# Kernel optimization log

Hardware: AMD Instinct MI355X
Metric: run time of the kernel (lower is better)

## Reference

```python
import jax, jax.numpy as jnp
import numpy as np

B, N, D, K, NUM_CLASSES = 8, 2048, 256, 8, 32
BN_EPS = 1e-5


def l2norm(x):
    return x / jnp.maximum(jnp.linalg.norm(x, axis=-1, keepdims=True), 1e-12)


def mlp2(x, W1, b1, W2, b2):
    # get_mlp([3, 32, D]): Linear -> ReLU -> Linear -> ReLU
    return jax.nn.relu(jax.nn.relu(x @ W1 + b1) @ W2 + b2)


def bn(x, g, b):
    # training-mode BatchNorm1d over all edges (flattened leading dims)
    ax = tuple(range(x.ndim - 1))
    m = jnp.mean(x, axis=ax, keepdims=True)
    v = jnp.var(x, axis=ax, keepdims=True)
    return (x - m) * jax.lax.rsqrt(v + BN_EPS) * g + b


def setup_inputs() -> dict:
    key = jax.random.key(0)
    ks = jax.random.split(key, 24)
    p = lambda i, shape: jax.random.normal(ks[i], shape, jnp.float32) * 0.05
    class_table = p(0, (NUM_CLASSES, D)).at[0].set(0.0)  # padding_idx=0
    return dict(
        class_idx=jax.random.randint(ks[1], (B, N), 0, NUM_CLASSES),
        colors=jax.random.uniform(ks[2], (B, N, 3), jnp.float32),
        positions=jax.random.normal(ks[3], (B, N, 3), jnp.float32),
        class_table=class_table,
        pos_W1=p(4, (3, 32)), pos_b1=p(5, (32,)),
        pos_W2=p(6, (32, D)), pos_b2=p(7, (D,)),
        col_W1=p(8, (3, 32)), col_b1=p(9, (32,)),
        col_W2=p(10, (32, D)), col_b2=p(11, (D,)),
        merge_W=p(12, (3 * D, D)), merge_b=p(13, (D,)),
        g_W1=p(14, (2 * D, D)), g_b1=p(15, (D,)),
        g_g1=jnp.ones((D,), jnp.float32), g_be1=jnp.zeros((D,), jnp.float32),
        g_W2=p(16, (D, D)), g_b2=p(17, (D,)),
        g_g2=jnp.ones((D,), jnp.float32), g_be2=jnp.zeros((D,), jnp.float32),
        lin_W1=p(18, (D, D)), lin_b1=p(19, (D,)),
        lin_W2=p(20, (D, D)), lin_b2=p(21, (D,)),
    )


def reference(class_idx, colors, positions, class_table,
              pos_W1, pos_b1, pos_W2, pos_b2,
              col_W1, col_b1, col_W2, col_b2,
              merge_W, merge_b,
              g_W1, g_b1, g_g1, g_be1, g_W2, g_b2, g_g2, g_be2,
              lin_W1, lin_b1, lin_W2, lin_b2):
    # --- per-object feature embeddings, each L2-normalized ---
    ce = l2norm(class_table[class_idx])                                   # [B,N,D]
    col = l2norm(mlp2(colors, col_W1, col_b1, col_W2, col_b2))            # [B,N,D]
    pos = l2norm(mlp2(positions, pos_W1, pos_b1, pos_W2, pos_b2))         # [B,N,D]
    x = jax.nn.relu(jnp.concatenate([ce, col, pos], -1) @ merge_W + merge_b)  # [B,N,D]
    # --- dynamic kNN in feature space, per sample (self edge included) ---
    sq = jnp.sum(x * x, -1)                                               # [B,N]
    d = sq[:, :, None] + sq[:, None, :] - 2.0 * jnp.einsum('bid,bjd->bij', x, x)
    _, idx = jax.lax.top_k(-jax.lax.stop_gradient(d), K)                  # [B,N,K]
    xj = jax.vmap(lambda e, i: e[i])(x, idx)                              # [B,N,K,D]
    xi = jnp.broadcast_to(x[:, :, None, :], xj.shape)
    e = jnp.concatenate([xi, xj - xi], -1)                                # [B,N,K,2D]
    # --- edge MLP [2D,D,D] with BN, max aggregation over neighbors ---
    h = bn(jax.nn.relu(e @ g_W1 + g_b1), g_g1, g_be1)
    h = bn(jax.nn.relu(h @ g_W2 + g_b2), g_g2, g_be2)
    node = jnp.max(h, axis=2)                                             # [B,N,D]
    pooled = jnp.max(node, axis=1)                                        # global_max_pool -> [B,D]
    out = jax.nn.relu(jax.nn.relu(pooled @ lin_W1 + lin_b1) @ lin_W2 + lin_b2)
    return l2norm(out)
```

## Files before the change

kernel.cpp:

```cpp
#include <hip/hip_runtime.h>
#include <math.h>

#define BB 8
#define NN 2048
#define DD 256
#define KNN 8
#define NPTS (BB*NN)
#define NEDGE (NPTS*KNN)
#define BN_EPS 1e-5f
#define NSH 64
#define PSH 32

#define OFF_X      0
#define OFF_FEAT   (OFF_X + NPTS*DD)
#define OFF_STATS  (OFF_FEAT + NPTS*3*DD)
#define OFF_PMAXS  (OFF_STATS + NSH*1024)
#define OFF_SQ     (OFF_PMAXS + PSH*BB*DD)
#define OFF_PMINS  (OFF_SQ + NPTS)
#define OFF_IDX    (OFF_PMINS + PSH*BB*DD)
#define OFF_U      (OFF_IDX + NEDGE)
#define OFF_V      (OFF_U + NPTS*DD)
#define OFF_W2BF   (OFF_V + NPTS*DD)
#define OFF_BIASP  (OFF_W2BF + 32768)
#define OFF_XHI    (OFF_BIASP + DD)
#define OFF_XLO    (OFF_XHI + NPTS*DD/2)
#define OFF_MWH    (OFF_XLO + NPTS*DD/2)
#define OFF_MWL    (OFF_MWH + 98304)
#define OFF_WUH    (OFF_MWL + 98304)
#define OFF_WUL    (OFF_WUH + 32768)
#define OFF_WBH    (OFF_WUL + 32768)
#define OFF_WBL    (OFF_WBH + 32768)

typedef __attribute__((ext_vector_type(8))) short bf16x8;
typedef __attribute__((ext_vector_type(4))) float f32x4;

__device__ __forceinline__ unsigned short f2bf(float f) {
  unsigned int u = __float_as_uint(f);
  u += 0x7FFF + ((u >> 16) & 1);
  return (unsigned short)(u >> 16);
}
__device__ __forceinline__ float bf2f(unsigned short h) {
  return __uint_as_float((unsigned int)h << 16);
}

__global__ __launch_bounds__(256) void prepk(
    const int* __restrict__ cls, const float* __restrict__ colors, const float* __restrict__ positions,
    const float* __restrict__ ctab,
    const float* __restrict__ pW1, const float* __restrict__ pb1, const float* __restrict__ pW2, const float* __restrict__ pb2,
    const float* __restrict__ cW1, const float* __restrict__ cb1, const float* __restrict__ cW2, const float* __restrict__ cb2,
    unsigned short* __restrict__ feathi, unsigned short* __restrict__ featlo,
    const float* __restrict__ mW,
    unsigned short* __restrict__ mwh, unsigned short* __restrict__ mwl,
    const float* __restrict__ gW1,
    unsigned short* __restrict__ Wuh, unsigned short* __restrict__ Wul,
    unsigned short* __restrict__ Wbh, unsigned short* __restrict__ Wbl)
{
  __shared__ float wbuf[4][64];
  int bx = blockIdx.x;
  int tid = threadIdx.x;
  if (bx < 4096) {
    int wv = tid >> 6, lane = tid & 63;
    int p = bx*4 + wv;
    if (lane < 32) {
      float c0 = colors[p*3+0], c1 = colors[p*3+1], c2 = colors[p*3+2];
      wbuf[wv][lane] = fmaxf(c0*cW1[lane] + c1*cW1[32+lane] + c2*cW1[64+lane] + cb1[lane], 0.f);
    } else {
      int l = lane - 32;
      float q0 = positions[p*3+0], q1 = positions[p*3+1], q2 = positions[p*3+2];
      wbuf[wv][32+l] = fmaxf(q0*pW1[l] + q1*pW1[32+l] + q2*pW1[64+l] + pb1[l], 0.f);
    }
    __syncthreads();
    int c = lane*4;
    float4 ce4 = *(const float4*)&ctab[(size_t)cls[p]*DD + c];
    float4 col4 = *(const float4*)&cb2[c];
    float4 pos4 = *(const float4*)&pb2[c];
    #pragma unroll
    for (int k = 0; k < 32; k++) {
      float ch = wbuf[wv][k], ph = wbuf[wv][32+k];
      float4 cw = *(const float4*)&cW2[k*DD + c];
      float4 pw = *(const float4*)&pW2[k*DD + c];
      col4.x += ch*cw.x; col4.y += ch*cw.y; col4.z += ch*cw.z; col4.w += ch*cw.w;
      pos4.x += ph*pw.x; pos4.y += ph*pw.y; pos4.z += ph*pw.z; pos4.w += ph*pw.w;
    }
    col4.x = fmaxf(col4.x, 0.f); col4.y = fmaxf(col4.y, 0.f);
    col4.z = fmaxf(col4.z, 0.f); col4.w = fmaxf(col4.w, 0.f);
    pos4.x = fmaxf(pos4.x, 0.f); pos4.y = fmaxf(pos4.y, 0.f);
    pos4.z = fmaxf(pos4.z, 0.f); pos4.w = fmaxf(pos4.w, 0.f);
    float sce  = ce4.x*ce4.x + ce4.y*ce4.y + ce4.z*ce4.z + ce4.w*ce4.w;
    float scol = col4.x*col4.x + col4.y*col4.y + col4.z*col4.z + col4.w*col4.w;
    float spos = pos4.x*pos4.x + pos4.y*pos4.y + pos4.z*pos4.z + pos4.w*pos4.w;
    #pragma unroll
    for (int m = 1; m <= 32; m <<= 1) {
      sce  += __shfl_xor(sce,  m, 64);
      scol += __shfl_xor(scol, m, 64);
      spos += __shfl_xor(spos, m, 64);
    }
    float ice = 1.f / fmaxf(sqrtf(sce),  1e-12f);
    float icl = 1.f / fmaxf(sqrtf(scol), 1e-12f);
    float ips = 1.f / fmaxf(sqrtf(spos), 1e-12f);
    float o[3][4] = {
      {ce4.x*ice,  ce4.y*ice,  ce4.z*ice,  ce4.w*ice},
      {col4.x*icl, col4.y*icl, col4.z*icl, col4.w*icl},
      {pos4.x*ips, pos4.y*ips, pos4.z*ips, pos4.w*ips}
    };
    #pragma unroll
    for (int sgm = 0; sgm < 3; sgm++) {
      unsigned short h[4], l[4];
      #pragma unroll
      for (int cc = 0; cc < 4; cc++) {
        h[cc] = f2bf(o[sgm][cc]);
        l[cc] = f2bf(o[sgm][cc] - bf2f(h[cc]));
      }
      size_t off = (size_t)p*768 + sgm*256 + c;
      *(uint2*)&feathi[off] = make_uint2((unsigned)h[0] | ((unsigned)h[1] << 16),
                                         (unsigned)h[2] | ((unsigned)h[3] << 16));
      *(uint2*)&featlo[off] = make_uint2((unsigned)l[0] | ((unsigned)l[1] << 16),
                                         (unsigned)l[2] | ((unsigned)l[3] << 16));
    }
  } else if (bx < 4096 + 768) {
    int k = bx - 4096;
    int n = tid;
    float wgt = mW[(size_t)k*DD + n];
    unsigned short h = f2bf(wgt);
    mwh[(size_t)n*768 + k] = h;
    mwl[(size_t)n*768 + k] = f2bf(wgt - bf2f(h));
  } else {
    int k = bx - (4096 + 768);
    int n = tid;
    float t = gW1[(size_t)k*DD + n];
    float b = gW1[(size_t)(k + DD)*DD + n];
    float wu = t - b;
    unsigned short uh = f2bf(wu), bh = f2bf(b);
    Wuh[(size_t)n*DD + k] = uh;
    Wul[(size_t)n*DD + k] = f2bf(wu - bf2f(uh));
    Wbh[(size_t)n*DD + k] = bh;
    Wbl[(size_t)n*DD + k] = f2bf(b - bf2f(bh));
  }
}

__global__ __launch_bounds__(256) void gemm768(
    const unsigned short* __restrict__ feathi, const unsigned short* __restrict__ featlo,
    const unsigned short* __restrict__ mwh, const unsigned short* __restrict__ mwl,
    const float* __restrict__ mb,
    float* __restrict__ sqo,
    unsigned short* __restrict__ xhi, unsigned short* __restrict__ xlo)
{
  __shared__ float wSh[128*18];
  __shared__ float wSl[128*18];
  int tid = threadIdx.x;
  int w = tid >> 6, lane = tid & 63;
  int m = lane & 15, quad = lane >> 4;
  int rowbase = blockIdx.x * 64;
  int colbase = blockIdx.y * 128;
  size_t aoff = (size_t)(rowbase + w*16 + m)*768;
  int srow = tid >> 1;
  int sseg = (tid & 1) * 2;
  f32x4 acc[8];
  #pragma unroll
  for (int t = 0; t < 8; t++) acc[t] = (f32x4){0.f, 0.f, 0.f, 0.f};
  #pragma unroll 1
  for (int c = 0; c < 24; c++) {
    int k0 = c*32 + quad*8;
    bf16x8 ah = *(const bf16x8*)(feathi + aoff + k0);
    bf16x8 al = *(const bf16x8*)(featlo + aoff + k0);
    const float* wrh = (const float*)(mwh + (size_t)(colbase + srow)*768 + c*32);
    const float* wrl = (const float*)(mwl + (size_t)(colbase + srow)*768 + c*32);
    float4 wh0 = *(const float4*)(wrh + sseg*4);
    float4 wh1 = *(const float4*)(wrh + (sseg+1)*4);
    float4 wl0 = *(const float4*)(wrl + sseg*4);
    float4 wl1 = *(const float4*)(wrl + (sseg+1)*4);
    __syncthreads();
    *(float4*)&wSh[srow*18 + sseg*4]     = wh0;
    *(float4*)&wSh[srow*18 + (sseg+1)*4] = wh1;
    *(float4*)&wSl[srow*18 + sseg*4]     = wl0;
    *(float4*)&wSl[srow*18 + (sseg+1)*4] = wl1;
    __syncthreads();
    #pragma unroll
    for (int nt = 0; nt < 8; nt++) {
      bf16x8 bh = *(const bf16x8*)&wSh[(nt*16 + m)*18 + quad*4];
      bf16x8 bl = *(const bf16x8*)&wSl[(nt*16 + m)*18 + quad*4];
      acc[nt] = __builtin_amdgcn_mfma_f32_16x16x32_bf16(ah, bh, acc[nt], 0, 0, 0);
      acc[nt] = __builtin_amdgcn_mfma_f32_16x16x32_bf16(ah, bl, acc[nt], 0, 0, 0);
      acc[nt] = __builtin_amdgcn_mfma_f32_16x16x32_bf16(al, bh, acc[nt], 0, 0, 0);
    }
  }
  float sqp[4] = {0.f, 0.f, 0.f, 0.f};
  #pragma unroll
  for (int nt = 0; nt < 8; nt++) {
    int col = colbase + nt*16 + m;
    float bp = mb[col];
    #pragma unroll
    for (int r = 0; r < 4; r++) {
      float o = fmaxf(acc[nt][r] + bp, 0.f);
      int row = rowbase + w*16 + quad*4 + r;
      unsigned short h = f2bf(o);
      xhi[(size_t)row*DD + col] = h;
      xlo[(size_t)row*DD + col] = f2bf(o - bf2f(h));
      sqp[r] += o*o;
    }
  }
  #pragma unroll
  for (int r = 0; r < 4; r++) {
    #pragma unroll
    for (int mm = 1; mm <= 8; mm <<= 1) sqp[r] += __shfl_xor(sqp[r], mm, 64);
  }
  if (m == 0) {
    #pragma unroll
    for (int r = 0; r < 4; r++)
      atomicAdd(&sqo[rowbase + w*16 + quad*4 + r], sqp[r]);
  }
}

__global__ __launch_bounds__(256) void knnuv(
    const unsigned short* __restrict__ xhi, const unsigned short* __restrict__ xlo,
    const float* __restrict__ sq,
    float* __restrict__ pdg, int* __restrict__ pjg,
    const unsigned short* __restrict__ Wuh, const unsigned short* __restrict__ Wul,
    const unsigned short* __restrict__ Wbh, const unsigned short* __restrict__ Wbl,
    float* __restrict__ U, float* __restrict__ V)
{
  __shared__ float smem[4736];
  int bx = blockIdx.x;
  int tid = threadIdx.x;
  int w = tid >> 6, lane = tid & 63;
  int m = lane & 15, quad = lane >> 4;
  if ((bx & 1) == 0) {
    int kid = bx >> 1;
    float* jh = smem;
    float* jl = smem + 2304;
    float (*dt)[65] = (float(*)[65])smem;
    float* sqI = smem + 4608;
    float* sqJ = smem + 4672;
    int q  = kid & 3;
    int it = (kid >> 2) & 31;
    int bb = kid >> 7;
    int ibase = it * 64;
    const unsigned short* xhb = xhi + (size_t)bb*NN*DD;
    const unsigned short* xlb = xlo + (size_t)bb*NN*DD;
    const float* sqb = sq + (size_t)bb*NN;
    int selrow = tid & 63, selseg = tid >> 6;
    size_t aoff = (size_t)(ibase + w*16 + m)*DD;
    int srow = tid >> 2;
    int sseg = tid & 3;
    bf16x8 ahr[8], alr[8];
    #pragma unroll
    for (int c = 0; c < 8; c++) {
      int k0 = c*32 + quad*8;
      ahr[c] = *(const bf16x8*)(xhb + aoff + k0);
      alr[c] = *(const bf16x8*)(xlb + aoff + k0);
    }
    float bd[8]; int bj[8];
    #pragma unroll
    for (int s = 0; s < 8; s++) { bd[s] = 3.4e38f; bj[s] = 0; }
    if (tid < 64) sqI[tid] = sqb[ibase + tid];
    #pragma unroll 1
    for (int jt = 0; jt < 8; jt++) {
      int jbase = q*512 + jt*64;
      if (tid < 64) sqJ[tid] = sqb[jbase + tid];
      f32x4 acc[4];
      #pragma unroll
      for (int t = 0; t < 4; t++) acc[t] = (f32x4){0.f, 0.f, 0.f, 0.f};
      #pragma unroll
      for (int c2 = 0; c2 < 4; c2++) {
        size_t gb = (size_t)(jbase + srow)*DD + c2*64;
        float4 h0 = *(const float4*)((const float*)(xhb + gb) + sseg*4);
        float4 h1 = *(const float4*)((const float*)(xhb + gb) + (sseg+4)*4);
        float4 l0 = *(const float4*)((const float*)(xlb + gb) + sseg*4);
        float4 l1 = *(const float4*)((const float*)(xlb + gb) + (sseg+4)*4);
        __syncthreads();
        *(float4*)&jh[srow*36 + sseg*4]     = h0;
        *(float4*)&jh[srow*36 + (sseg+4)*4] = h1;
        *(float4*)&jl[srow*36 + sseg*4]     = l0;
        *(float4*)&jl[srow*36 + (sseg+4)*4] = l1;
        __syncthreads();
        #pragma unroll
        for (int kk = 0; kk < 2; kk++) {
          bf16x8 ah = ahr[c2*2 + kk];
          bf16x8 al = alr[c2*2 + kk];
          int lofs = kk*16 + quad*4;
          #pragma unroll
          for (int nt = 0; nt < 4; nt++) {
            int r = nt*16 + m;
            bf16x8 bh = *(const bf16x8*)&jh[r*36 + lofs];
            bf16x8 bl = *(const bf16x8*)&jl[r*36 + lofs];
            acc[nt] = __builtin_amdgcn_mfma_f32_16x16x32_bf16(ah, bh, acc[nt], 0, 0, 0);
            acc[nt] = __builtin_amdgcn_mfma_f32_16x16x32_bf16(ah, bl, acc[nt], 0, 0, 0);
            acc[nt] = __builtin_amdgcn_mfma_f32_16x16x32_bf16(al, bh, acc[nt], 0, 0, 0);
          }
        }
      }
      __syncthreads();
      #pragma unroll
      for (int nt = 0; nt < 4; nt++) {
        int col = nt*16 + m;
        float sj = sqJ[col];
        #pragma unroll
        for (int r = 0; r < 4; r++) {
          int rowl = w*16 + quad*4 + r;
          dt[rowl][col] = sqI[rowl] + sj - 2.f*acc[nt][r];
        }
      }
      __syncthreads();
      int cb = selseg*16;
      #pragma unroll
      for (int s = 0; s < 16; s++) {
        float dv = dt[selrow][cb + s];
        if (dv < bd[7]) {
          bd[7] = dv; bj[7] = jbase + cb + s;
          #pragma unroll
          for (int t = 7; t >= 1; t--) {
            if (bd[t] < bd[t-1]) {
              float td = bd[t]; bd[t] = bd[t-1]; bd[t-1] = td;
              int   tj = bj[t]; bj[t] = bj[t-1]; bj[t-1] = tj;
            }
          }
        }
      }
    }
    __syncthreads();
    float* pdl = &smem[0];
    int*   pjl = (int*)&smem[2048];
    #pragma unroll
    for (int s = 0; s < 8; s++) {
      pdl[tid*8 + s] = bd[s];
      pjl[tid*8 + s] = bj[s];
    }
    __syncthreads();
    if (tid < 64) {
      float md[8]; int mj[8];
      #pragma unroll
      for (int s = 0; s < 8; s++) { md[s] = 3.4e38f; mj[s] = 0; }
      #pragma unroll 1
      for (int g = 0; g < 4; g++) {
        int base = (g*64 + tid)*8;
        #pragma unroll
        for (int s = 0; s < 8; s++) {
          float dv = pdl[base + s];
          if (dv < md[7]) {
            md[7] = dv; mj[7] = pjl[base + s];
            #pragma unroll
            for (int t = 7; t >= 1; t--) {
              if (md[t] < md[t-1]) {
                float td = md[t]; md[t] = md[t-1]; md[t-1] = td;
                int   tj = mj[t]; mj[t] = mj[t-1]; mj[t-1] = tj;
              }
            }
          }
        }
      }
      size_t gbase = ((size_t)(bb*NN + ibase + tid))*32 + (size_t)q*8;
      #pragma unroll
      for (int s = 0; s < 8; s++) {
        pdg[gbase + s] = md[s];
        pjg[gbase + s] = bb*NN + mj[s];
      }
    }
  } else {
    int gid = bx >> 1;
    float* wSh = smem;
    float* wSl = smem + 2304;
    int rowbase = (gid & 255) * 64;
    int yy = gid >> 8;
    int uv = yy >> 1;
    int colbase = (yy & 1) * 128;
    const unsigned short* Wh = uv ? Wbh : Wuh;
    const unsigned short* Wl = uv ? Wbl : Wul;
    float* Out = uv ? V : U;
    size_t aoff = (size_t)(rowbase + w*16 + m)*DD;
    int srow = tid >> 1;
    int sseg = (tid & 1) * 2;
    f32x4 acc[8];
    #pragma unroll
    for (int t = 0; t < 8; t++) acc[t] = (f32x4){0.f, 0.f, 0.f, 0.f};
    #pragma unroll 1
    for (int c = 0; c < 8; c++) {
      int k0 = c*32 + quad*8;
      bf16x8 ah = *(const bf16x8*)(xhi + aoff + k0);
      bf16x8 al = *(const bf16x8*)(xlo + aoff + k0);
      const float* wrh = (const float*)(Wh + (size_t)(colbase + srow)*DD + c*32);
      const float* wrl = (const float*)(Wl + (size_t)(colbase + srow)*DD + c*32);
      float4 wh0 = *(const float4*)(wrh + sseg*4);
      float4 wh1 = *(const float4*)(wrh + (sseg+1)*4);
      float4 wl0 = *(const float4*)(wrl + sseg*4);
      float4 wl1 = *(const float4*)(wrl + (sseg+1)*4);
      __syncthreads();
      *(float4*)&wSh[srow*18 + sseg*4]     = wh0;
      *(float4*)&wSh[srow*18 + (sseg+1)*4] = wh1;
      *(float4*)&wSl[srow*18 + sseg*4]     = wl0;
      *(float4*)&wSl[srow*18 + (sseg+1)*4] = wl1;
      __syncthreads();
      #pragma unroll
      for (int nt = 0; nt < 8; nt++) {
        bf16x8 bh = *(const bf16x8*)&wSh[(nt*16 + m)*18 + quad*4];
        bf16x8 bl = *(const bf16x8*)&wSl[(nt*16 + m)*18 + quad*4];
        acc[nt] = __builtin_amdgcn_mfma_f32_16x16x32_bf16(ah, bh, acc[nt], 0, 0, 0);
        acc[nt] = __builtin_amdgcn_mfma_f32_16x16x32_bf16(ah, bl, acc[nt], 0, 0, 0);
        acc[nt] = __builtin_amdgcn_mfma_f32_16x16x32_bf16(al, bh, acc[nt], 0, 0, 0);
      }
    }
    #pragma unroll
    for (int nt = 0; nt < 8; nt++) {
      int col = colbase + nt*16 + m;
      #pragma unroll
      for (int r = 0; r < 4; r++) {
        int row = rowbase + w*16 + quad*4 + r;
        Out[(size_t)row*DD + col] = acc[nt][r];
      }
    }
  }
}

__global__ __launch_bounds__(256) void knnmerge(const float* __restrict__ pdg, const int* __restrict__ pjg,
                                                int* __restrict__ idxg)
{
  int p = blockIdx.x*256 + threadIdx.x;
  float md[8]; int mj[8];
  #pragma unroll
  for (int s = 0; s < 8; s++) { md[s] = 3.4e38f; mj[s] = 0; }
  size_t base = (size_t)p*32;
  #pragma unroll 1
  for (int s = 0; s < 32; s++) {
    float dv = pdg[base + s];
    if (dv < md[7]) {
      md[7] = dv; mj[7] = pjg[base + s];
      #pragma unroll
      for (int t = 7; t >= 1; t--) {
        if (md[t] < md[t-1]) {
          float td = md[t]; md[t] = md[t-1]; md[t-1] = td;
          int   tj = mj[t]; mj[t] = mj[t-1]; mj[t-1] = tj;
        }
      }
    }
  }
  #pragma unroll
  for (int s = 0; s < 8; s++) idxg[(size_t)p*8 + s] = mj[s];
}

__global__ __launch_bounds__(256) void bn1stats(const float* __restrict__ u, const float* __restrict__ v,
    const int* __restrict__ idxg, const float* __restrict__ b1, float* __restrict__ stats)
{
  __shared__ int jL[128];
  int c = threadIdx.x;
  int n0 = blockIdx.x * 16;
  if (c < 128) jL[c] = idxg[(size_t)n0*8 + c];
  __syncthreads();
  float b1c = b1[c];
  float s = 0.f, s2 = 0.f;
  #pragma unroll 1
  for (int n = 0; n < 16; n++) {
    float uc = u[(size_t)(n0 + n)*DD + c];
    #pragma unroll
    for (int e = 0; e < 8; e++) {
      int j = jL[n*8 + e];
      float h = fmaxf(uc + v[(size_t)j*DD + c] + b1c, 0.f);
      s += h; s2 += h*h;
    }
  }
  int row = blockIdx.x & (NSH - 1);
  atomicAdd(&stats[row*1024 + c], s);
  atomicAdd(&stats[row*1024 + 256 + c], s2);
}

__global__ __launch_bounds__(256) void prep2(const float* __restrict__ stats, const float* __restrict__ g1,
    const float* __restrict__ be1, const float* __restrict__ gW2, const float* __restrict__ gb2,
    unsigned short* __restrict__ w2bf, float* __restrict__ biasp)
{
  __shared__ float s1L[256], t1L[256];
  int tid = threadIdx.x;
  const float inv = 1.f / (float)NEDGE;
  float sm = 0.f, sq2 = 0.f;
  #pragma unroll 1
  for (int r = 0; r < NSH; r++) {
    sm  += stats[r*1024 + tid];
    sq2 += stats[r*1024 + 256 + tid];
  }
  float m = sm * inv;
  float var = sq2*inv - m*m;
  float s1 = g1[tid] / sqrtf(var + BN_EPS);
  s1L[tid] = s1; t1L[tid] = be1[tid] - m*s1;
  __syncthreads();
  float bacc = gb2[tid];
  for (int k = 0; k < DD; k++) {
    float w = gW2[k*DD + tid];
    w2bf[(size_t)tid*DD + k] = f2bf(s1L[k]*w);
    bacc += t1L[k]*w;
  }
  biasp[tid] = bacc;
}

__global__ __launch_bounds__(256) void edgek(
    const float* __restrict__ u, const float* __restrict__ v, const int* __restrict__ idxg,
    const float* __restrict__ b1, const unsigned short* __restrict__ w2bf,
    const float* __restrict__ biasp,
    float* __restrict__ pmaxs, float* __restrict__ pmins, float* __restrict__ stats)
{
  __shared__ float wS[128*18];
  int tid = threadIdx.x;
  int w = tid >> 6, lane = tid & 63;
  int m = lane & 15, quad = lane >> 4;
  int rowbase = blockIdx.x * 64;
  int colbase = blockIdx.y * 128;
  int edge = rowbase + w*16 + m;
  int iu = edge >> 3;
  int jv = idxg[edge];
  const float* urow = u + (size_t)iu*DD;
  const float* vrow = v + (size_t)jv*DD;
  int srow = tid >> 1;
  int sseg = (tid & 1) * 2;
  f32x4 acc[8];
  #pragma unroll
  for (int t = 0; t < 8; t++) acc[t] = (f32x4){0.f, 0.f, 0.f, 0.f};
  #pragma unroll 1
  for (int c = 0; c < 8; c++) {
    int k0 = c*32 + quad*8;
    float4 ua = *(const float4*)(urow + k0);
    float4 ub = *(const float4*)(urow + k0 + 4);
    float4 va = *(const float4*)(vrow + k0);
    float4 vb = *(const float4*)(vrow + k0 + 4);
    float4 ba = *(const float4*)(b1 + k0);
    float4 bb = *(const float4*)(b1 + k0 + 4);
    const float* wrow = (const float*)(w2bf + (size_t)(colbase + srow)*DD + c*32);
    float4 wreg0 = *(const float4*)(wrow + sseg*4);
    float4 wreg1 = *(const float4*)(wrow + (sseg+1)*4);
    float h0 = fmaxf(ua.x+va.x+ba.x, 0.f);
    float h1 = fmaxf(ua.y+va.y+ba.y, 0.f);
    float h2 = fmaxf(ua.z+va.z+ba.z, 0.f);
    float h3 = fmaxf(ua.w+va.w+ba.w, 0.f);
    float h4 = fmaxf(ub.x+vb.x+bb.x, 0.f);
    float h5 = fmaxf(ub.y+vb.y+bb.y, 0.f);
    float h6 = fmaxf(ub.z+vb.z+bb.z, 0.f);
    float h7 = fmaxf(ub.w+vb.w+bb.w, 0.f);
    union { bf16x8 v8; unsigned short s[8]; } af;
    af.s[0] = f2bf(h0); af.s[1] = f2bf(h1); af.s[2] = f2bf(h2); af.s[3] = f2bf(h3);
    af.s[4] = f2bf(h4); af.s[5] = f2bf(h5); af.s[6] = f2bf(h6); af.s[7] = f2bf(h7);
    __syncthreads();
    *(float4*)&wS[srow*18 + sseg*4]     = wreg0;
    *(float4*)&wS[srow*18 + (sseg+1)*4] = wreg1;
    __syncthreads();
    #pragma unroll
    for (int nt = 0; nt < 8; nt++) {
      bf16x8 bf = *(const bf16x8*)&wS[(nt*16 + m)*18 + quad*4];
      acc[nt] = __builtin_amdgcn_mfma_f32_16x16x32_bf16(af.v8, bf, acc[nt], 0, 0, 0);
    }
  }
  float* redS = wS;
  float* redQ = wS + 512;
  float* redM = wS + 1024;
  float* redN = wS + 1536;
  float mxr[8], mnr[8], ssr[8], sqr[8];
  #pragma unroll
  for (int nt = 0; nt < 8; nt++) {
    int col = nt*16 + m;
    float bp = biasp[colbase + col];
    float r0 = fmaxf(acc[nt].x + bp, 0.f);
    float r1 = fmaxf(acc[nt].y + bp, 0.f);
    float r2 = fmaxf(acc[nt].z + bp, 0.f);
    float r3 = fmaxf(acc[nt].w + bp, 0.f);
    float mx = fmaxf(fmaxf(r0, r1), fmaxf(r2, r3));
    float mn = fminf(fminf(r0, r1), fminf(r2, r3));
    float ss = r0 + r1 + r2 + r3;
    float s2 = r0*r0 + r1*r1 + r2*r2 + r3*r3;
    mx = fmaxf(mx, __shfl_xor(mx, 16, 64));
    mx = fmaxf(mx, __shfl_xor(mx, 32, 64));
    mn = fminf(mn, __shfl_xor(mn, 16, 64));
    mn = fminf(mn, __shfl_xor(mn, 32, 64));
    ss += __shfl_xor(ss, 16, 64);
    ss += __shfl_xor(ss, 32, 64);
    s2 += __shfl_xor(s2, 16, 64);
    s2 += __shfl_xor(s2, 32, 64);
    mxr[nt] = mx; mnr[nt] = mn; ssr[nt] = ss; sqr[nt] = s2;
  }
  __syncthreads();
  if (quad == 0) {
    #pragma unroll
    for (int nt = 0; nt < 8; nt++) {
      int col = nt*16 + m;
      redS[w*128 + col] = ssr[nt];
      redQ[w*128 + col] = sqr[nt];
      redM[w*128 + col] = mxr[nt];
      redN[w*128 + col] = mnr[nt];
    }
  }
  __syncthreads();
  if (tid < 128) {
    float ts  = redS[tid] + redS[128+tid] + redS[256+tid] + redS[384+tid];
    float tq  = redQ[tid] + redQ[128+tid] + redQ[256+tid] + redQ[384+tid];
    float mxc = fmaxf(fmaxf(redM[tid], redM[128+tid]), fmaxf(redM[256+tid], redM[384+tid]));
    float mnc = fminf(fminf(redN[tid], redN[128+tid]), fminf(redN[256+tid], redN[384+tid]));
    int row = blockIdx.x & (NSH - 1);
    atomicAdd(&stats[row*1024 + 512 + colbase + tid], ts);
    atomicAdd(&stats[row*1024 + 768 + colbase + tid], tq);
    int b  = blockIdx.x >> 8;
    int sh = blockIdx.x & (PSH - 1);
    atomicMax((int*)&pmaxs[((size_t)sh*BB + b)*DD + colbase + tid], __float_as_int(mxc));
    atomicMin((int*)&pmins[((size_t)sh*BB + b)*DD + colbase + tid], __float_as_int(mnc));
  }
}

__global__ __launch_bounds__(256) void finalk(const float* __restrict__ pmaxs, const float* __restrict__ pmins,
    const float* __restrict__ stats, const float* __restrict__ g2, const float* __restrict__ be2,
    const float* __restrict__ W1, const float* __restrict__ b1,
    const float* __restrict__ W2, const float* __restrict__ b2,
    float* __restrict__ out)
{
  __shared__ float pl[256];
  __shared__ float hl[256];
  __shared__ float red[4];
  int c = threadIdx.x;
  int b = blockIdx.x;
  const float inv = 1.f / (float)NEDGE;
  float sm = 0.f, sq2 = 0.f;
  #pragma unroll 1
  for (int r = 0; r < NSH; r++) {
    sm  += stats[r*1024 + 512 + c];
    sq2 += stats[r*1024 + 768 + c];
  }
  float m = sm * inv;
  float var = sq2*inv - m*m;
  float s2 = g2[c] / sqrtf(var + BN_EPS);
  float t2 = be2[c] - m*s2;
  float mx = -3.4e38f, mn = 3.4e38f;
  #pragma unroll 1
  for (int s = 0; s < PSH; s++) {
    mx = fmaxf(mx, pmaxs[((size_t)s*BB + b)*DD + c]);
    mn = fminf(mn, pmins[((size_t)s*BB + b)*DD + c]);
  }
  pl[c] = (s2 >= 0.f) ? s2*mx + t2 : s2*mn + t2;
  __syncthreads();
  float h = b1[c];
  #pragma unroll 4
  for (int k = 0; k < 256; k++) h += pl[k]*W1[k*256 + c];
  hl[c] = fmaxf(h, 0.f);
  __syncthreads();
  float o = b2[c];
  #pragma unroll 4
  for (int k = 0; k < 256; k++) o += hl[k]*W2[k*256 + c];
  o = fmaxf(o, 0.f);
  float s = o*o;
  #pragma unroll
  for (int mm = 1; mm <= 32; mm <<= 1) s += __shfl_xor(s, mm, 64);
  if ((c & 63) == 0) red[c >> 6] = s;
  __syncthreads();
  float tot = red[0] + red[1] + red[2] + red[3];
  out[b*256 + c] = o / fmaxf(sqrtf(tot), 1e-12f);
}

extern "C" void kernel_launch(void* const* d_in, const int* in_sizes, int n_in,
                              void* d_out, int out_size, void* d_ws, size_t ws_size,
                              hipStream_t stream) {
  (void)in_sizes; (void)n_in; (void)out_size; (void)ws_size;
  const int*   cls       = (const int*)  d_in[0];
  const float* colors    = (const float*)d_in[1];
  const float* positions = (const float*)d_in[2];
  const float* ctab      = (const float*)d_in[3];
  const float* pW1 = (const float*)d_in[4];
  const float* pb1 = (const float*)d_in[5];
  const float* pW2 = (const float*)d_in[6];
  const float* pb2 = (const float*)d_in[7];
  const float* cW1 = (const float*)d_in[8];
  const float* cb1 = (const float*)d_in[9];
  const float* cW2 = (const float*)d_in[10];
  const float* cb2 = (const float*)d_in[11];
  const float* mW  = (const float*)d_in[12];
  const float* mb  = (const float*)d_in[13];
  const float* gW1 = (const float*)d_in[14];
  const float* gb1 = (const float*)d_in[15];
  const float* gg1 = (const float*)d_in[16];
  const float* gbe1= (const float*)d_in[17];
  const float* gW2 = (const float*)d_in[18];
  const float* gb2 = (const float*)d_in[19];
  const float* gg2 = (const float*)d_in[20];
  const float* gbe2= (const float*)d_in[21];
  const float* lW1 = (const float*)d_in[22];
  const float* lb1 = (const float*)d_in[23];
  const float* lW2 = (const float*)d_in[24];
  const float* lb2 = (const float*)d_in[25];
  float* out = (float*)d_out;

  float* wsf   = (float*)d_ws;
  unsigned short* feathi = (unsigned short*)(wsf + OFF_FEAT);
  unsigned short* featlo = feathi + (size_t)NPTS*768;
  float* sq    = wsf + OFF_SQ;
  int*   idxg  = (int*)(wsf + OFF_IDX);
  float* u     = wsf + OFF_U;
  float* v     = wsf + OFF_V;
  unsigned short* w2bf = (unsigned short*)(wsf + OFF_W2BF);
  float* biasp = wsf + OFF_BIASP;
  unsigned short* xhi = (unsigned short*)(wsf + OFF_XHI);
  unsigned short* xlo = (unsigned short*)(wsf + OFF_XLO);
  unsigned short* mwh = (unsigned short*)(wsf + OFF_MWH);
  unsigned short* mwl = (unsigned short*)(wsf + OFF_MWL);
  unsigned short* Wuh = (unsigned short*)(wsf + OFF_WUH);
  unsigned short* Wul = (unsigned short*)(wsf + OFF_WUL);
  unsigned short* Wbh = (unsigned short*)(wsf + OFF_WBH);
  unsigned short* Wbl = (unsigned short*)(wsf + OFF_WBL);
  float* stats = wsf + OFF_STATS;
  float* pmaxs = wsf + OFF_PMAXS;
  float* pmins = wsf + OFF_PMINS;
  float* pdg   = wsf + OFF_FEAT;
  int*   pjg   = (int*)(wsf + OFF_FEAT + (size_t)NPTS*32);

  hipMemsetAsync(stats, 0, (NSH*1024 + PSH*BB*DD + NPTS)*sizeof(float), stream);
  hipMemsetAsync(pmins, 0x7f, PSH*BB*DD*sizeof(float), stream);

  prepk<<<4096 + 768 + 256, 256, 0, stream>>>(cls, colors, positions, ctab,
                                              pW1, pb1, pW2, pb2, cW1, cb1, cW2, cb2,
                                              feathi, featlo, mW, mwh, mwl,
                                              gW1, Wuh, Wul, Wbh, Wbl);
  gemm768<<<dim3(NPTS/64, 2), 256, 0, stream>>>(feathi, featlo, mwh, mwl, mb, sq, xhi, xlo);
  knnuv<<<2048, 256, 0, stream>>>(xhi, xlo, sq, pdg, pjg, Wuh, Wul, Wbh, Wbl, u, v);
  knnmerge<<<NPTS/256, 256, 0, stream>>>(pdg, pjg, idxg);
  bn1stats<<<NPTS/16, 256, 0, stream>>>(u, v, idxg, gb1, stats);
  prep2<<<1, 256, 0, stream>>>(stats, gg1, gbe1, gW2, gb2, w2bf, biasp);
  edgek<<<dim3(NEDGE/64, 2), 256, 0, stream>>>(u, v, idxg, gb1, w2bf, biasp, pmaxs, pmins, stats);
  finalk<<<BB, 256, 0, stream>>>(pmaxs, pmins, stats, gg2, gbe2, lW1, lb1, lW2, lb2, out);
}
```

Before: 605.9 us.

## Split fused kNN/UV kernel into separate kNN and UV GEMM kernels

Separates the previously interleaved kernel, which alternated kNN distance/top-k blocks with U/V projection GEMM blocks, into two kernels launched in sequence. The UV GEMM now runs after knnmerge. This removes the branch-divergent fused layout, so each kernel can get its own register and LDS allocation and occupancy. The cost is an extra launch and losing the concurrency between the two workloads.

```diff
diff --git a/kernel.cpp b/kernel.cpp
--- a/kernel.cpp
+++ b/kernel.cpp
@@ -211,201 +211,202 @@
   }
 }
 
-__global__ __launch_bounds__(256) void knnuv(
+__global__ __launch_bounds__(256) void gemmuv(
     const unsigned short* __restrict__ xhi, const unsigned short* __restrict__ xlo,
-    const float* __restrict__ sq,
-    float* __restrict__ pdg, int* __restrict__ pjg,
     const unsigned short* __restrict__ Wuh, const unsigned short* __restrict__ Wul,
     const unsigned short* __restrict__ Wbh, const unsigned short* __restrict__ Wbl,
     float* __restrict__ U, float* __restrict__ V)
 {
-  __shared__ float smem[4736];
-  int bx = blockIdx.x;
+  __shared__ float wSh[128*18];
+  __shared__ float wSl[128*18];
   int tid = threadIdx.x;
   int w = tid >> 6, lane = tid & 63;
   int m = lane & 15, quad = lane >> 4;
-  if ((bx & 1) == 0) {
-    int kid = bx >> 1;
-    float* jh = smem;
-    float* jl = smem + 2304;
-    float (*dt)[65] = (float(*)[65])smem;
-    float* sqI = smem + 4608;
-    float* sqJ = smem + 4672;
-    int q  = kid & 3;
-    int it = (kid >> 2) & 31;
-    int bb = kid >> 7;
-    int ibase = it * 64;
-    const unsigned short* xhb = xhi + (size_t)bb*NN*DD;
-    const unsigned short* xlb = xlo + (size_t)bb*NN*DD;
-    const float* sqb = sq + (size_t)bb*NN;
-    int selrow = tid & 63, selseg = tid >> 6;
-    size_t aoff = (size_t)(ibase + w*16 + m)*DD;
-    int srow = tid >> 2;
-    int sseg = tid & 3;
-    bf16x8 ahr[8], alr[8];
-    #pragma unroll
-    for (int c = 0; c < 8; c++) {
-      int k0 = c*32 + quad*8;
-      ahr[c] = *(const bf16x8*)(xhb + aoff + k0);
-      alr[c] = *(const bf16x8*)(xlb + aoff + k0);
-    }
-    float bd[8]; int bj[8];
-    #pragma unroll
-    for (int s = 0; s < 8; s++) { bd[s] = 3.4e38f; bj[s] = 0; }
-    if (tid < 64) sqI[tid] = sqb[ibase + tid];
-    #pragma unroll 1
-    for (int jt = 0; jt < 8; jt++) {
-      int jbase = q*512 + jt*64;
-      if (tid < 64) sqJ[tid] = sqb[jbase + tid];
-      f32x4 acc[4];
+  int rowbase = blockIdx.x * 64;
+  int uv = blockIdx.y >> 1;
+  int colbase = (blockIdx.y & 1) * 128;
+  const unsigned short* Wh = uv ? Wbh : Wuh;
+  const unsigned short* Wl = uv ? Wbl : Wul;
+  float* Out = uv ? V : U;
+  size_t aoff = (size_t)(rowbase + w*16 + m)*DD;
+  int srow = tid >> 1;
+  int sseg = (tid & 1) * 2;
+  f32x4 acc[8];
+  #pragma unroll
+  for (int t = 0; t < 8; t++) acc[t] = (f32x4){0.f, 0.f, 0.f, 0.f};
+  #pragma unroll 1
+  for (int c = 0; c < 8; c++) {
+    int k0 = c*32 + quad*8;
+    bf16x8 ah = *(const bf16x8*)(xhi + aoff + k0);
+    bf16x8 al = *(const bf16x8*)(xlo + aoff + k0);
+    const float* wrh = (const float*)(Wh + (size_t)(colbase + srow)*DD + c*32);
+    const float* wrl = (const float*)(Wl + (size_t)(colbase + srow)*DD + c*32);
+    float4 wh0 = *(const float4*)(wrh + sseg*4);
+    float4 wh1 = *(const float4*)(wrh + (sseg+1)*4);
+    float4 wl0 = *(const float4*)(wrl + sseg*4);
+    float4 wl1 = *(const float4*)(wrl + (sseg+1)*4);
+    __syncthreads();
+    *(float4*)&wSh[srow*18 + sseg*4]     = wh0;
+    *(float4*)&wSh[srow*18 + (sseg+1)*4] = wh1;
+    *(float4*)&wSl[srow*18 + sseg*4]     = wl0;
+    *(float4*)&wSl[srow*18 + (sseg+1)*4] = wl1;
+    __syncthreads();
+    #pragma unroll
+    for (int nt = 0; nt < 8; nt++) {
+      bf16x8 bh = *(const bf16x8*)&wSh[(nt*16 + m)*18 + quad*4];
+      bf16x8 bl = *(const bf16x8*)&wSl[(nt*16 + m)*18 + quad*4];
+      acc[nt] = __builtin_amdgcn_mfma_f32_16x16x32_bf16(ah, bh, acc[nt], 0, 0, 0);
+      acc[nt] = __builtin_amdgcn_mfma_f32_16x16x32_bf16(ah, bl, acc[nt], 0, 0, 0);
+      acc[nt] = __builtin_amdgcn_mfma_f32_16x16x32_bf16(al, bh, acc[nt], 0, 0, 0);
+    }
+  }
+  #pragma unroll
+  for (int nt = 0; nt < 8; nt++) {
+    int col = colbase + nt*16 + m;
+    #pragma unroll
+    for (int r = 0; r < 4; r++) {
+      int row = rowbase + w*16 + quad*4 + r;
+      Out[(size_t)row*DD + col] = acc[nt][r];
+    }
+  }
+}
+
+__global__ __launch_bounds__(256) void knnk(
+    const unsigned short* __restrict__ xhi, const unsigned short* __restrict__ xlo,
+    const float* __restrict__ sq,
+    float* __restrict__ pdg, int* __restrict__ pjg)
+{
+  __shared__ float smem[4736];
+  float* jh = smem;
+  float* jl = smem + 2304;
+  float (*dt)[65] = (float(*)[65])smem;
+  float* sqI = smem + 4608;
+  float* sqJ = smem + 4672;
+  int tid = threadIdx.x;
+  int q  = blockIdx.x & 3;
+  int it = (blockIdx.x >> 2) & 31;
+  int bb = blockIdx.x >> 7;
+  int ibase = it * 64;
+  const unsigned short* xhb = xhi + (size_t)bb*NN*DD;
+  const unsigned short* xlb = xlo + (size_t)bb*NN*DD;
+  const float* sqb = sq + (size_t)bb*NN;
+  int w = tid >> 6, lane = tid & 63;
+  int m = lane & 15, quad = lane >> 4;
+  int selrow = tid & 63, selseg = tid >> 6;
+  size_t aoff = (size_t)(ibase + w*16 + m)*DD;
+  int srow = tid >> 2;
+  int sseg = tid & 3;
+  bf16x8 ahr[8], alr[8];
+  #pragma unroll
+  for (int c = 0; c < 8; c++) {
+    int k0 = c*32 + quad*8;
+    ahr[c] = *(const bf16x8*)(xhb + aoff + k0);
+    alr[c] = *(const bf16x8*)(xlb + aoff + k0);
+  }
+  float bd[8]; int bj[8];
+  #pragma unroll
+  for (int s = 0; s < 8; s++) { bd[s] = 3.4e38f; bj[s] = 0; }
+  if (tid < 64) sqI[tid] = sqb[ibase + tid];
+  #pragma unroll 1
+  for (int jt = 0; jt < 8; jt++) {
+    int jbase = q*512 + jt*64;
+    if (tid < 64) sqJ[tid] = sqb[jbase + tid];
+    f32x4 acc[4];
+    #pragma unroll
+    for (int t = 0; t < 4; t++) acc[t] = (f32x4){0.f, 0.f, 0.f, 0.f};
+    #pragma unroll
+    for (int c2 = 0; c2 < 4; c2++) {
+      size_t gb = (size_t)(jbase + srow)*DD + c2*64;
+      float4 h0 = *(const float4*)((const float*)(xhb + gb) + sseg*4);
+      float4 h1 = *(const float4*)((const float*)(xhb + gb) + (sseg+4)*4);
+      float4 l0 = *(const float4*)((const float*)(xlb + gb) + sseg*4);
+      float4 l1 = *(const float4*)((const float*)(xlb + gb) + (sseg+4)*4);
+      __syncthreads();
+      *(float4*)&jh[srow*36 + sseg*4]     = h0;
+      *(float4*)&jh[srow*36 + (sseg+4)*4] = h1;
+      *(float4*)&jl[srow*36 + sseg*4]     = l0;
+      *(float4*)&jl[srow*36 + (sseg+4)*4] = l1;
+      __syncthreads();
       #pragma unroll
-      for (int t = 0; t < 4; t++) acc[t] = (f32x4){0.f, 0.f, 0.f, 0.f};
+      for (int kk = 0; kk < 2; kk++) {
+        bf16x8 ah = ahr[c2*2 + kk];
+        bf16x8 al = alr[c2*2 + kk];
+        int lofs = kk*16 + quad*4;
+        #pragma unroll
+        for (int nt = 0; nt < 4; nt++) {
+          int r = nt*16 + m;
+          bf16x8 bh = *(const bf16x8*)&jh[r*36 + lofs];
+          bf16x8 bl = *(const bf16x8*)&jl[r*36 + lofs];
+          acc[nt] = __builtin_amdgcn_mfma_f32_16x16x32_bf16(ah, bh, acc[nt], 0, 0, 0);
+          acc[nt] = __builtin_amdgcn_mfma_f32_16x16x32_bf16(ah, bl, acc[nt], 0, 0, 0);
+          acc[nt] = __builtin_amdgcn_mfma_f32_16x16x32_bf16(al, bh, acc[nt], 0, 0, 0);
+        }
+      }
+    }
+    __syncthreads();
+    #pragma unroll
+    for (int nt = 0; nt < 4; nt++) {
+      int col = nt*16 + m;
+      float sj = sqJ[col];
       #pragma unroll
-      for (int c2 = 0; c2 < 4; c2++) {
-        size_t gb = (size_t)(jbase + srow)*DD + c2*64;
-        float4 h0 = *(const float4*)((const float*)(xhb + gb) + sseg*4);
-        float4 h1 = *(const float4*)((const float*)(xhb + gb) + (sseg+4)*4);
-        float4 l0 = *(const float4*)((const float*)(xlb + gb) + sseg*4);
-        float4 l1 = *(const float4*)((const float*)(xlb + gb) + (sseg+4)*4);
-        __syncthreads();
-        *(float4*)&jh[srow*36 + sseg*4]     = h0;
-        *(float4*)&jh[srow*36 + (sseg+4)*4] = h1;
-        *(float4*)&jl[srow*36 + sseg*4]     = l0;
-        *(float4*)&jl[srow*36 + (sseg+4)*4] = l1;
-        __syncthreads();
+      for (int r = 0; r < 4; r++) {
+        int rowl = w*16 + quad*4 + r;
+        dt[rowl][col] = sqI[rowl] + sj - 2.f*acc[nt][r];
+      }
+    }
+    __syncthreads();
+    int cb = selseg*16;
+    #pragma unroll
+    for (int s = 0; s < 16; s++) {
+      float dv = dt[selrow][cb + s];
+      if (dv < bd[7]) {
+        bd[7] = dv; bj[7] = jbase + cb + s;
         #pragma unroll
-        for (int kk = 0; kk < 2; kk++) {
-          bf16x8 ah = ahr[c2*2 + kk];
-          bf16x8 al = alr[c2*2 + kk];
-          int lofs = kk*16 + quad*4;
-          #pragma unroll
-          for (int nt = 0; nt < 4; nt++) {
-            int r = nt*16 + m;
-            bf16x8 bh = *(const bf16x8*)&jh[r*36 + lofs];
-            bf16x8 bl = *(const bf16x8*)&jl[r*36 + lofs];
-            acc[nt] = __builtin_amdgcn_mfma_f32_16x16x32_bf16(ah, bh, acc[nt], 0, 0, 0);
-            acc[nt] = __builtin_amdgcn_mfma_f32_16x16x32_bf16(ah, bl, acc[nt], 0, 0, 0);
-            acc[nt] = __builtin_amdgcn_mfma_f32_16x16x32_bf16(al, bh, acc[nt], 0, 0, 0);
+        for (int t = 7; t >= 1; t--) {
+          if (bd[t] < bd[t-1]) {
+            float td = bd[t]; bd[t] = bd[t-1]; bd[t-1] = td;
+            int   tj = bj[t]; bj[t] = bj[t-1]; bj[t-1] = tj;
           }
         }
       }
-      __syncthreads();
+    }
+  }
+  __syncthreads();
+  float* pdl = &smem[0];
+  int*   pjl = (int*)&smem[2048];
+  #pragma unroll
+  for (int s = 0; s < 8; s++) {
+    pdl[tid*8 + s] = bd[s];
+    pjl[tid*8 + s] = bj[s];
+  }
+  __syncthreads();
+  if (tid < 64) {
+    float md[8]; int mj[8];
+    #pragma unroll
+    for (int s = 0; s < 8; s++) { md[s] = 3.4e38f; mj[s] = 0; }
+    #pragma unroll 1
+    for (int g = 0; g < 4; g++) {
+      int base = (g*64 + tid)*8;
       #pragma unroll
-      for (int nt = 0; nt < 4; nt++) {
-        int col = nt*16 + m;
-        float sj = sqJ[col];
-        #pragma unroll
-        for (int r = 0; r < 4; r++) {
-          int rowl = w*16 + quad*4 + r;
-          dt[rowl][col] = sqI[rowl] + sj - 2.f*acc[nt][r];
-        }
-      }
-      __syncthreads();
-      int cb = selseg*16;
-      #pragma unroll
-      for (int s = 0; s < 16; s++) {
-        float dv = dt[selrow][cb + s];
-        if (dv < bd[7]) {
-          bd[7] = dv; bj[7] = jbase + cb + s;
+      for (int s = 0; s < 8; s++) {
+        float dv = pdl[base + s];
+        if (dv < md[7]) {
+          md[7] = dv; mj[7] = pjl[base + s];
           #pragma unroll
           for (int t = 7; t >= 1; t--) {
-            if (bd[t] < bd[t-1]) {
-              float td = bd[t]; bd[t] = bd[t-1]; bd[t-1] = td;
-              int   tj = bj[t]; bj[t] = bj[t-1]; bj[t-1] = tj;
+            if (md[t] < md[t-1]) {
+              float td = md[t]; md[t] = md[t-1]; md[t-1] = td;
+              int   tj = mj[t]; mj[t] = mj[t-1]; mj[t-1] = tj;
             }
           }
         }
       }
     }
-    __syncthreads();
-    float* pdl = &smem[0];
-    int*   pjl = (int*)&smem[2048];
+    size_t gbase = ((size_t)(bb*NN + ibase + tid))*32 + (size_t)q*8;
     #pragma unroll
     for (int s = 0; s < 8; s++) {
-      pdl[tid*8 + s] = bd[s];
-      pjl[tid*8 + s] = bj[s];
-    }
-    __syncthreads();
-    if (tid < 64) {
-      float md[8]; int mj[8];
-      #pragma unroll
-      for (int s = 0; s < 8; s++) { md[s] = 3.4e38f; mj[s] = 0; }
-      #pragma unroll 1
-      for (int g = 0; g < 4; g++) {
-        int base = (g*64 + tid)*8;
-        #pragma unroll
-        for (int s = 0; s < 8; s++) {
-          float dv = pdl[base + s];
-          if (dv < md[7]) {
-            md[7] = dv; mj[7] = pjl[base + s];
-            #pragma unroll
-            for (int t = 7; t >= 1; t--) {
-              if (md[t] < md[t-1]) {
-                float td = md[t]; md[t] = md[t-1]; md[t-1] = td;
-                int   tj = mj[t]; mj[t] = mj[t-1]; mj[t-1] = tj;
-              }
-            }
-          }
-        }
-      }
-      size_t gbase = ((size_t)(bb*NN + ibase + tid))*32 + (size_t)q*8;
-      #pragma unroll
-      for (int s = 0; s < 8; s++) {
-        pdg[gbase + s] = md[s];
-        pjg[gbase + s] = bb*NN + mj[s];
-      }
-    }
-  } else {
-    int gid = bx >> 1;
-    float* wSh = smem;
-    float* wSl = smem + 2304;
-    int rowbase = (gid & 255) * 64;
-    int yy = gid >> 8;
-    int uv = yy >> 1;
-    int colbase = (yy & 1) * 128;
-    const unsigned short* Wh = uv ? Wbh : Wuh;
-    const unsigned short* Wl = uv ? Wbl : Wul;
-    float* Out = uv ? V : U;
-    size_t aoff = (size_t)(rowbase + w*16 + m)*DD;
-    int srow = tid >> 1;
-    int sseg = (tid & 1) * 2;
-    f32x4 acc[8];
-    #pragma unroll
-    for (int t = 0; t < 8; t++) acc[t] = (f32x4){0.f, 0.f, 0.f, 0.f};
-    #pragma unroll 1
-    for (int c = 0; c < 8; c++) {
-      int k0 = c*32 + quad*8;
-      bf16x8 ah = *(const bf16x8*)(xhi + aoff + k0);
-      bf16x8 al = *(const bf16x8*)(xlo + aoff + k0);
-      const float* wrh = (const float*)(Wh + (size_t)(colbase + srow)*DD + c*32);
-      const float* wrl = (const float*)(Wl + (size_t)(colbase + srow)*DD + c*32);
-      float4 wh0 = *(const float4*)(wrh + sseg*4);
-      float4 wh1 = *(const float4*)(wrh + (sseg+1)*4);
-      float4 wl0 = *(const float4*)(wrl + sseg*4);
-      float4 wl1 = *(const float4*)(wrl + (sseg+1)*4);
-      __syncthreads();
-      *(float4*)&wSh[srow*18 + sseg*4]     = wh0;
-      *(float4*)&wSh[srow*18 + (sseg+1)*4] = wh1;
-      *(float4*)&wSl[srow*18 + sseg*4]     = wl0;
-      *(float4*)&wSl[srow*18 + (sseg+1)*4] = wl1;
-      __syncthreads();
-      #pragma unroll
-      for (int nt = 0; nt < 8; nt++) {
-        bf16x8 bh = *(const bf16x8*)&wSh[(nt*16 + m)*18 + quad*4];
-        bf16x8 bl = *(const bf16x8*)&wSl[(nt*16 + m)*18 + quad*4];
-        acc[nt] = __builtin_amdgcn_mfma_f32_16x16x32_bf16(ah, bh, acc[nt], 0, 0, 0);
-        acc[nt] = __builtin_amdgcn_mfma_f32_16x16x32_bf16(ah, bl, acc[nt], 0, 0, 0);
-        acc[nt] = __builtin_amdgcn_mfma_f32_16x16x32_bf16(al, bh, acc[nt], 0, 0, 0);
-      }
-    }
-    #pragma unroll
-    for (int nt = 0; nt < 8; nt++) {
-      int col = colbase + nt*16 + m;
-      #pragma unroll
-      for (int r = 0; r < 4; r++) {
-        int row = rowbase + w*16 + quad*4 + r;
-        Out[(size_t)row*DD + col] = acc[nt][r];
-      }
+      pdg[gbase + s] = md[s];
+      pjg[gbase + s] = bb*NN + mj[s];
     }
   }
 }
@@ -708,8 +709,9 @@
                                               feathi, featlo, mW, mwh, mwl,
                                               gW1, Wuh, Wul, Wbh, Wbl);
   gemm768<<<dim3(NPTS/64, 2), 256, 0, stream>>>(feathi, featlo, mwh, mwl, mb, sq, xhi, xlo);
-  knnuv<<<2048, 256, 0, stream>>>(xhi, xlo, sq, pdg, pjg, Wuh, Wul, Wbh, Wbl, u, v);
+  knnk<<<BB*32*4, 256, 0, stream>>>(xhi, xlo, sq, pdg, pjg);
   knnmerge<<<NPTS/256, 256, 0, stream>>>(pdg, pjg, idxg);
+  gemmuv<<<dim3(NPTS/64, 4), 256, 0, stream>>>(xhi, xlo, Wuh, Wul, Wbh, Wbl, u, v);
   bn1stats<<<NPTS/16, 256, 0, stream>>>(u, v, idxg, gb1, stats);
   prep2<<<1, 256, 0, stream>>>(stats, gg1, gbe1, gW2, gb2, w2bf, biasp);
   edgek<<<dim3(NEDGE/64, 2), 256, 0, stream>>>(u, v, idxg, gb1, w2bf, biasp, pmaxs, pmins, stats);
```

After: 518.7 us. 1.17x faster.
